# Kernel tuning notes

Measured on AMD Instinct MI355X. Metric: run time of the kernel, lower is better.

## Reference

```python
import jax, jax.numpy as jnp
import numpy as np
from jax import lax

# ReplicationPad1d (left,right) per kernel size, matching Python round((ks-1)/2)
PADS = {2: (0, 1), 3: (1, 1), 6: (2, 3), 12: (6, 5)}

B, N, T, C, OC, E = 8, 1024, 64, 16, 16, 16384


def setup_inputs() -> dict:
    key = jax.random.key(0)
    ks = jax.random.split(key, 16)

    def wn(k, shape, fan_in):
        return jax.random.normal(k, shape, jnp.float32) / jnp.sqrt(jnp.float32(fan_in))

    inp = {
        "x": jax.random.normal(ks[0], (B, N, T, C), jnp.float32),
        "edge_index": jax.random.randint(ks[1], (2, E), 0, N, dtype=jnp.int32),
        # temporal conv branches (Conv1d: [out_ch, in_ch, ks])
        "w_t2": wn(ks[2], (OC, C, 2), C * 2), "b_t2": jnp.zeros((OC,), jnp.float32),
        "w_t3": wn(ks[3], (OC, C, 3), C * 3), "b_t3": jnp.zeros((OC,), jnp.float32),
        "w_t6": wn(ks[4], (OC, C, 6), C * 6), "b_t6": jnp.zeros((OC,), jnp.float32),
        "w_t12": wn(ks[5], (OC, C, 12), C * 12), "b_t12": jnp.zeros((OC,), jnp.float32),
        # GCNConv: lin weight [out, in] (no bias in lin), separate bias
        "w_gcn": wn(ks[6], (OC, C), C), "b_gcn": jnp.zeros((OC,), jnp.float32),
        # slin: Linear(T -> T)
        "w_slin": wn(ks[7], (T, T), T), "b_slin": jnp.zeros((T,), jnp.float32),
    }
    return inp


def reference(x, edge_index, w_t2, b_t2, w_t3, b_t3, w_t6, b_t6, w_t12, b_t12,
              w_gcn, b_gcn, w_slin, b_slin):
    Bd, Nd, Td, Cd = x.shape
    # ---- temporal multi-scale Conv1d branches ----
    xt = x.reshape(Bd * Nd, Td, Cd).transpose(0, 2, 1)  # [BN, C, T]
    outs = []
    for w, b in ((w_t2, b_t2), (w_t3, b_t3), (w_t6, b_t6), (w_t12, b_t12)):
        kern = w.shape[-1]
        l, r = PADS[kern]
        xp = jnp.pad(xt, ((0, 0), (0, 0), (l, r)), mode="edge")  # replication pad
        y = lax.conv_general_dilated(xp, w, (1,), "VALID",
                                     dimension_numbers=("NCH", "OIH", "NCH"))
        outs.append((y + b[None, :, None]).transpose(0, 2, 1))  # [BN, T, OC]
    out_t = jnp.concatenate(outs, axis=-1).reshape(Bd, Nd, Td, -1)  # [B,N,T,4*OC]

    # ---- GCNConv spatial branch (gather-transform-scatter) ----
    xs = x.transpose(0, 2, 1, 3)                         # [B,T,N,C]
    xl = jnp.einsum("btnc,oc->btno", xs, w_gcn)          # [B,T,N,OC]
    row, col = edge_index[0], edge_index[1]
    deg = jnp.zeros((Nd,), x.dtype).at[col].add(1.0) + 1.0  # +1 self loop
    dinv = lax.rsqrt(deg)
    norm = dinv[row] * dinv[col]                         # [E]
    msgs = xl[:, :, row, :] * norm[None, None, :, None]  # gather [B,T,E,OC]
    agg = jnp.zeros_like(xl).at[:, :, col, :].add(msgs)  # scatter-add
    agg = agg + (dinv * dinv)[None, None, :, None] * xl + b_gcn  # self loops + bias

    xs_out = agg.transpose(0, 2, 3, 1)                   # [B,N,OC,T]
    xs_out = jnp.einsum("bnot,st->bnos", xs_out, w_slin) + b_slin
    xs_out = xs_out.transpose(0, 1, 3, 2)                # [B,N,T,OC]

    return jnp.tanh(jnp.concatenate([out_t, xs_out], axis=-1))  # [B,N,T,embed_dim]
```

## Files before the change

kernel.cpp:

```cpp
#include <hip/hip_runtime.h>
#include <hip/hip_bf16.h>

#define BB  8
#define NN  1024
#define TT  64
#define CC  16
#define OCC 16
#define EE  16384
#define CHO 80

typedef float  f32x4  __attribute__((ext_vector_type(4)));
typedef __bf16 bf16x8 __attribute__((ext_vector_type(8)));

static __device__ __forceinline__ float tanh_fast(float v) {
    float e = __expf(2.0f * v);
    return 1.0f - 2.0f * __builtin_amdgcn_rcpf(e + 1.0f);
}
static __device__ __forceinline__ unsigned pk_bf16(float a, float b) {
    unsigned short lo = __builtin_bit_cast(unsigned short, (__bf16)a);
    unsigned short hi = __builtin_bit_cast(unsigned short, (__bf16)b);
    return (unsigned)lo | ((unsigned)hi << 16);
}
static __device__ __forceinline__ float bflo(unsigned u) { return __uint_as_float(u << 16); }
static __device__ __forceinline__ float bfhi(unsigned u) { return __uint_as_float(u & 0xFFFF0000u); }

static __device__ __forceinline__ void acc8(float* ac, int base, float w, float4 v) {
    unsigned ux = __float_as_uint(v.x), uy = __float_as_uint(v.y);
    unsigned uz = __float_as_uint(v.z), uw = __float_as_uint(v.w);
    ac[base + 0] = fmaf(w, bflo(ux), ac[base + 0]);
    ac[base + 1] = fmaf(w, bfhi(ux), ac[base + 1]);
    ac[base + 2] = fmaf(w, bflo(uy), ac[base + 2]);
    ac[base + 3] = fmaf(w, bfhi(uy), ac[base + 3]);
    ac[base + 4] = fmaf(w, bflo(uz), ac[base + 4]);
    ac[base + 5] = fmaf(w, bfhi(uz), ac[base + 5]);
    ac[base + 6] = fmaf(w, bflo(uw), ac[base + 6]);
    ac[base + 7] = fmaf(w, bfhi(uw), ac[base + 7]);
}


__global__ __launch_bounds__(1024) void k_prep(
    const int* __restrict__ ei, const float* __restrict__ x,
    const float* __restrict__ w2,  const float* __restrict__ b2,
    const float* __restrict__ w3,  const float* __restrict__ b3,
    const float* __restrict__ w6,  const float* __restrict__ b6,
    const float* __restrict__ w12, const float* __restrict__ b12,
    const float* __restrict__ wg,  const float* __restrict__ bg,
    const float* __restrict__ wsl,
    int* __restrict__ offg, int* __restrict__ cntg, float* __restrict__ dinvg,
    int* __restrict__ src, float* __restrict__ wE,
    float* __restrict__ wgT, float* __restrict__ bgp, float* __restrict__ bcat,
    __bf16* __restrict__ wslh, __bf16* __restrict__ wsll, __bf16* __restrict__ wtg,
    __bf16* __restrict__ xb) {
    int tid = threadIdx.x, bid = blockIdx.x;
    const float* wsrc[4] = {w2, w3, w6, w12};
    const float* bsrc[4] = {b2, b3, b6, b12};
    const int ksA[4] = {2, 3, 6, 12};
    const int plA[4] = {0, 1, 2, 6};
    if (bid >= 14) {
        int e4 = (bid - 14) * 1024 + tid;
        float4 u = ((const float4*)x)[e4];
        uint2 w;
        w.x = pk_bf16(u.x, u.y);
        w.y = pk_bf16(u.z, u.w);
        ((uint2*)xb)[e4] = w;
        return;
    }
    if (bid == 13) {
        if (tid < 256) wgT[tid] = wg[(tid & 15) * CC + (tid >> 4)];
        else if (tid < 272) bgp[tid - 256] = bg[tid - 256];
        else if (tid < 336) { int j = tid - 272; bcat[j] = bsrc[j >> 4][j & 15]; }
        for (int e = tid; e < 4096; e += 1024) {
            float v = wsl[e];
            __bf16 h = (__bf16)v;
            wslh[e] = h;
            wsll[e] = (__bf16)(v - (float)h);
        }
        return;
    }
    if (bid != 0) {
        int e = (bid - 1) * 1024 + tid;
        int j = e / 192, kk = e - j * 192;
        int d = kk >> 4, c = kk & 15;
        int br = j >> 4, oc = j & 15;
        int k = d - 6 + plA[br];
        float v = (k >= 0 && k < ksA[br]) ? wsrc[br][oc * (CC * ksA[br]) + c * ksA[br] + k] : 0.0f;
        wtg[e] = (__bf16)v;
        return;
    }
    __shared__ int   h[NN];
    __shared__ int   sc[NN];
    __shared__ int   cur[NN];
    __shared__ float dl[NN];
    h[tid] = 0;
    __syncthreads();
    for (int e = tid; e < EE; e += 1024) atomicAdd(&h[ei[EE + e]], 1);
    __syncthreads();
    int v = h[tid];
    sc[tid] = v;
    __syncthreads();
    for (int d = 1; d < NN; d <<= 1) {
        int add = (tid >= d) ? sc[tid - d] : 0;
        __syncthreads();
        sc[tid] += add;
        __syncthreads();
    }
    int oex = sc[tid] - v;
    float dv = rsqrtf((float)v + 1.0f);
    offg[tid] = oex; cntg[tid] = v; dinvg[tid] = dv;
    cur[tid] = oex; dl[tid] = dv;
    __syncthreads();
    for (int e = tid; e < EE; e += 1024) {
        int r = ei[e], c = ei[EE + e];
        int i = atomicAdd(&cur[c], 1);
        src[i] = r;
        wE[i]  = dl[r] * dl[c];
    }
}


__global__ __launch_bounds__(256) void k_main(
    const __bf16* __restrict__ xb, const __bf16* __restrict__ wtg,
    const float* __restrict__ bcat,
    const int* __restrict__ off, const int* __restrict__ cnt,
    const int* __restrict__ src, const float* __restrict__ wE, const float* __restrict__ dinv,
    const float* __restrict__ wgT, const float* __restrict__ bgp,
    const __bf16* __restrict__ wslh, const __bf16* __restrict__ wsll,
    const float* __restrict__ bsl, float* __restrict__ out) {
    __shared__ __align__(16) char smem[18432];
    int tid = threadIdx.x;
    int wave = tid >> 6, lane = tid & 63;
    int l15 = lane & 15, g = lane >> 4;
    int bq = blockIdx.x & 7, nq = blockIdx.x >> 3;
    int n = nq * 4 + wave;
    const __bf16* xbb = xb + (size_t)bq * NN * (TT * CC);

    bf16x8 afr[6];
#pragma unroll
    for (int s = 0; s < 6; s++) {
        const __bf16* p = wtg + (wave * 16 + l15) * 192 + s * 32 + g * 8;
        afr[s] = __builtin_bit_cast(bf16x8, *(const float4*)p);
    }
    float4 bias = *(const float4*)(bcat + wave * 16 + g * 4);

    {
        int t = tid >> 2, c0 = (tid & 3) * 4;
#pragma unroll
        for (int node = 0; node < 4; node++) {
            __bf16* xsn = (__bf16*)(smem + node * 3648);
            uint2 w = *(const uint2*)(xbb + (size_t)(nq * 4 + node) * (TT * CC) + tid * 4);
            *(uint2*)(xsn + (t + 6) * 24 + c0) = w;
            if (t == 0) {
#pragma unroll
                for (int r = 0; r < 6; r++) *(uint2*)(xsn + r * 24 + c0) = w;
            }
            if (t == 63) {
#pragma unroll
                for (int r = 70; r < 76; r++) *(uint2*)(xsn + r * 24 + c0) = w;
            }
        }
    }
    __syncthreads();

    for (int node = 0; node < 4; node++) {
        const __bf16* xsn = (const __bf16*)(smem + node * 3648);
        size_t bn = (size_t)bq * NN + nq * 4 + node;
        f32x4 acc[4];
#pragma unroll
        for (int m = 0; m < 4; m++) acc[m] = (f32x4){bias.x, bias.y, bias.z, bias.w};
#pragma unroll
        for (int m = 0; m < 4; m++) {
#pragma unroll
            for (int s = 0; s < 6; s++) {
                const __bf16* p = xsn + (m * 16 + l15 + 2 * s + (g >> 1)) * 24 + (g & 1) * 8;
                bf16x8 b = __builtin_bit_cast(bf16x8, *(const float4*)p);
                acc[m] = __builtin_amdgcn_mfma_f32_16x16x32_bf16(afr[s], b, acc[m], 0, 0, 0);
            }
        }
#pragma unroll
        for (int m = 0; m < 4; m++) {
            float4 o;
            o.x = tanh_fast(acc[m][0]); o.y = tanh_fast(acc[m][1]);
            o.z = tanh_fast(acc[m][2]); o.w = tanh_fast(acc[m][3]);
            *(float4*)(out + (bn * TT + m * 16 + l15) * CHO + wave * 16 + g * 4) = o;
        }
    }

    float ac[16];
    {
        int o0 = off[n], cn_ = cnt[n];
        float d = dinv[n], d2 = d * d;
        const __bf16* st = xbb + (size_t)n * (TT * CC) + lane * 16;
        float4 s0 = *(const float4*)st;
        float4 s1 = *(const float4*)(st + 8);
        {
            unsigned ux = __float_as_uint(s0.x), uy = __float_as_uint(s0.y);
            unsigned uz = __float_as_uint(s0.z), uw = __float_as_uint(s0.w);
            ac[0] = d2 * bflo(ux); ac[1] = d2 * bfhi(ux);
            ac[2] = d2 * bflo(uy); ac[3] = d2 * bfhi(uy);
            ac[4] = d2 * bflo(uz); ac[5] = d2 * bfhi(uz);
            ac[6] = d2 * bflo(uw); ac[7] = d2 * bfhi(uw);
            ux = __float_as_uint(s1.x); uy = __float_as_uint(s1.y);
            uz = __float_as_uint(s1.z); uw = __float_as_uint(s1.w);
            ac[8]  = d2 * bflo(ux); ac[9]  = d2 * bfhi(ux);
            ac[10] = d2 * bflo(uy); ac[11] = d2 * bfhi(uy);
            ac[12] = d2 * bflo(uz); ac[13] = d2 * bfhi(uz);
            ac[14] = d2 * bflo(uw); ac[15] = d2 * bfhi(uw);
        }
        const int* srcp = src + o0;
        const float* wEp = wE + o0;
        int j = 0;
        for (; j + 4 <= cn_; j += 4) {
            int sA = srcp[j], sB = srcp[j + 1], sC = srcp[j + 2], sD = srcp[j + 3];
            float wA = wEp[j], wB = wEp[j + 1], wC = wEp[j + 2], wD = wEp[j + 3];
            const __bf16* pa = xbb + (size_t)sA * (TT * CC) + lane * 16;
            const __bf16* pb = xbb + (size_t)sB * (TT * CC) + lane * 16;
            const __bf16* pc = xbb + (size_t)sC * (TT * CC) + lane * 16;
            const __bf16* pd = xbb + (size_t)sD * (TT * CC) + lane * 16;
            float4 a0 = *(const float4*)pa, a1 = *(const float4*)(pa + 8);
            float4 b0 = *(const float4*)pb, b1 = *(const float4*)(pb + 8);
            float4 c0 = *(const float4*)pc, c1 = *(const float4*)(pc + 8);
            float4 d0 = *(const float4*)pd, d1 = *(const float4*)(pd + 8);
            acc8(ac, 0, wA, a0); acc8(ac, 8, wA, a1);
            acc8(ac, 0, wB, b0); acc8(ac, 8, wB, b1);
            acc8(ac, 0, wC, c0); acc8(ac, 8, wC, c1);
            acc8(ac, 0, wD, d0); acc8(ac, 8, wD, d1);
        }
        for (; j < cn_; j++) {
            int sA = srcp[j];
            float wA = wEp[j];
            const __bf16* pa = xbb + (size_t)sA * (TT * CC) + lane * 16;
            float4 a0 = *(const float4*)pa, a1 = *(const float4*)(pa + 8);
            acc8(ac, 0, wA, a0); acc8(ac, 8, wA, a1);
        }
    }

    float pv[16];
#pragma unroll
    for (int o = 0; o < 16; o++) {
        float p = bgp[o];
#pragma unroll
        for (int c = 0; c < 16; c++) p = fmaf(wgT[c * 16 + o], ac[c], p);
        pv[o] = p;
    }
    __syncthreads();

    {
        __bf16* xhn = (__bf16*)(smem + wave * 4608);
        __bf16* xln = (__bf16*)(smem + wave * 4608 + 2304);
#pragma unroll
        for (int o = 0; o < 16; o++) {
            __bf16 h = (__bf16)pv[o];
            xhn[o * 72 + lane] = h;
            xln[o * 72 + lane] = (__bf16)(pv[o] - (float)h);
        }
    }
    __syncthreads();

    int sglob = wave * 16 + l15;
    bf16x8 bh[2], bl[2];
#pragma unroll
    for (int k = 0; k < 2; k++) {
        bh[k] = __builtin_bit_cast(bf16x8, *(const float4*)(wslh + sglob * 64 + k * 32 + g * 8));
        bl[k] = __builtin_bit_cast(bf16x8, *(const float4*)(wsll + sglob * 64 + k * 32 + g * 8));
    }
    float bv = bsl[sglob];
    for (int node = 0; node < 4; node++) {
        const __bf16* xhn = (const __bf16*)(smem + node * 4608);
        const __bf16* xln = (const __bf16*)(smem + node * 4608 + 2304);
        f32x4 acc = (f32x4){bv, bv, bv, bv};
        bf16x8 ah[2], al[2];
#pragma unroll
        for (int k = 0; k < 2; k++) {
            ah[k] = __builtin_bit_cast(bf16x8, *(const float4*)(xhn + l15 * 72 + k * 32 + g * 8));
            al[k] = __builtin_bit_cast(bf16x8, *(const float4*)(xln + l15 * 72 + k * 32 + g * 8));
        }
#pragma unroll
        for (int k = 0; k < 2; k++) {
            acc = __builtin_amdgcn_mfma_f32_16x16x32_bf16(ah[k], bh[k], acc, 0, 0, 0);
            acc = __builtin_amdgcn_mfma_f32_16x16x32_bf16(al[k], bh[k], acc, 0, 0, 0);
            acc = __builtin_amdgcn_mfma_f32_16x16x32_bf16(ah[k], bl[k], acc, 0, 0, 0);
        }
        float4 o4;
        o4.x = tanh_fast(acc[0]); o4.y = tanh_fast(acc[1]);
        o4.z = tanh_fast(acc[2]); o4.w = tanh_fast(acc[3]);
        size_t bn = (size_t)bq * NN + nq * 4 + node;
        *(float4*)(out + (bn * TT + sglob) * CHO + 64 + g * 4) = o4;
    }
}


extern "C" void kernel_launch(void* const* d_in, const int* in_sizes, int n_in,
                              void* d_out, int out_size, void* d_ws, size_t ws_size,
                              hipStream_t stream) {
    const float* x   = (const float*)d_in[0];
    const int*   ei  = (const int*)d_in[1];
    const float* w2  = (const float*)d_in[2];
    const float* b2  = (const float*)d_in[3];
    const float* w3  = (const float*)d_in[4];
    const float* b3  = (const float*)d_in[5];
    const float* w6  = (const float*)d_in[6];
    const float* b6  = (const float*)d_in[7];
    const float* w12 = (const float*)d_in[8];
    const float* b12 = (const float*)d_in[9];
    const float* wg  = (const float*)d_in[10];
    const float* bg  = (const float*)d_in[11];
    const float* wsl = (const float*)d_in[12];
    const float* bsl = (const float*)d_in[13];
    float* out = (float*)d_out;

    char*   ws   = (char*)d_ws;
    int*    off  = (int*)(ws);
    int*    cnt  = (int*)(ws + 4096);
    float*  dinv = (float*)(ws + 8192);
    int*    src  = (int*)(ws + 12288);
    float*  wE   = (float*)(ws + 77824);
    float*  wgT  = (float*)(ws + 143360);
    float*  bgp  = (float*)(ws + 144384);
    float*  bcat = (float*)(ws + 144448);
    __bf16* wslh = (__bf16*)(ws + 144704);
    __bf16* wsll = (__bf16*)(ws + 152896);
    __bf16* wtg  = (__bf16*)(ws + 161088);
    __bf16* xb   = (__bf16*)(ws + 4194304);

    k_prep<<<2062, 1024, 0, stream>>>(ei, x, w2, b2, w3, b3, w6, b6, w12, b12, wg, bg, wsl,
                                      off, cnt, dinv, src, wE, wgT, bgp, bcat,
                                      wslh, wsll, wtg, xb);
    k_main<<<BB * NN / 4, 256, 0, stream>>>(xb, wtg, bcat, off, cnt, src, wE, dinv,
                                            wgT, bgp, wslh, wsll, bsl, out);
}
```

Before: 94.87 us.

## Specialize warps: run temporal conv and GCN gather concurrently in 512-thread blocks

Doubles the block to 8 waves and gives each group its own job. Waves 0-3 stage x and compute the temporal MFMA conv, while waves 4-7 each run one node's GCN neighbor gather and projection at the same time. Shared memory is split into separate buffers so the two phases no longer alias, and the slin MFMA stage is split across all 8 waves, two nodes each. The aim is to overlap latency-bound gather loads with conv compute, at the cost of higher per-block register and LDS pressure and possible imbalance between the two wave groups.

```diff
diff --git a/kernel.cpp b/kernel.cpp
--- a/kernel.cpp
+++ b/kernel.cpp
@@ -118,7 +118,7 @@
 }
 
 
-__global__ __launch_bounds__(256) void k_main(
+__global__ __launch_bounds__(512) void k_main(
     const __bf16* __restrict__ xb, const __bf16* __restrict__ wtg,
     const float* __restrict__ bcat,
     const int* __restrict__ off, const int* __restrict__ cnt,
@@ -126,137 +126,128 @@
     const float* __restrict__ wgT, const float* __restrict__ bgp,
     const __bf16* __restrict__ wslh, const __bf16* __restrict__ wsll,
     const float* __restrict__ bsl, float* __restrict__ out) {
-    __shared__ __align__(16) char smem[18432];
+    __shared__ __align__(16) __bf16 xs[4][76 * 24];
+    __shared__ __align__(16) __bf16 xh[4][16 * 72];
+    __shared__ __align__(16) __bf16 xl2[4][16 * 72];
     int tid = threadIdx.x;
-    int wave = tid >> 6, lane = tid & 63;
+    int wid = tid >> 6, lane = tid & 63;
     int l15 = lane & 15, g = lane >> 4;
     int bq = blockIdx.x & 7, nq = blockIdx.x >> 3;
-    int n = nq * 4 + wave;
     const __bf16* xbb = xb + (size_t)bq * NN * (TT * CC);
 
-    bf16x8 afr[6];
-#pragma unroll
-    for (int s = 0; s < 6; s++) {
-        const __bf16* p = wtg + (wave * 16 + l15) * 192 + s * 32 + g * 8;
-        afr[s] = __builtin_bit_cast(bf16x8, *(const float4*)p);
-    }
-    float4 bias = *(const float4*)(bcat + wave * 16 + g * 4);
-
-    {
+    if (wid < 4) {
         int t = tid >> 2, c0 = (tid & 3) * 4;
 #pragma unroll
         for (int node = 0; node < 4; node++) {
-            __bf16* xsn = (__bf16*)(smem + node * 3648);
             uint2 w = *(const uint2*)(xbb + (size_t)(nq * 4 + node) * (TT * CC) + tid * 4);
-            *(uint2*)(xsn + (t + 6) * 24 + c0) = w;
+            *(uint2*)(xs[node] + (t + 6) * 24 + c0) = w;
             if (t == 0) {
 #pragma unroll
-                for (int r = 0; r < 6; r++) *(uint2*)(xsn + r * 24 + c0) = w;
+                for (int r = 0; r < 6; r++) *(uint2*)(xs[node] + r * 24 + c0) = w;
             }
             if (t == 63) {
 #pragma unroll
-                for (int r = 70; r < 76; r++) *(uint2*)(xsn + r * 24 + c0) = w;
-            }
-        }
-    }
-    __syncthreads();
-
-    for (int node = 0; node < 4; node++) {
-        const __bf16* xsn = (const __bf16*)(smem + node * 3648);
-        size_t bn = (size_t)bq * NN + nq * 4 + node;
-        f32x4 acc[4];
-#pragma unroll
-        for (int m = 0; m < 4; m++) acc[m] = (f32x4){bias.x, bias.y, bias.z, bias.w};
-#pragma unroll
-        for (int m = 0; m < 4; m++) {
-#pragma unroll
-            for (int s = 0; s < 6; s++) {
-                const __bf16* p = xsn + (m * 16 + l15 + 2 * s + (g >> 1)) * 24 + (g & 1) * 8;
-                bf16x8 b = __builtin_bit_cast(bf16x8, *(const float4*)p);
-                acc[m] = __builtin_amdgcn_mfma_f32_16x16x32_bf16(afr[s], b, acc[m], 0, 0, 0);
-            }
-        }
-#pragma unroll
-        for (int m = 0; m < 4; m++) {
-            float4 o;
-            o.x = tanh_fast(acc[m][0]); o.y = tanh_fast(acc[m][1]);
-            o.z = tanh_fast(acc[m][2]); o.w = tanh_fast(acc[m][3]);
-            *(float4*)(out + (bn * TT + m * 16 + l15) * CHO + wave * 16 + g * 4) = o;
-        }
-    }
-
-    float ac[16];
-    {
-        int o0 = off[n], cn_ = cnt[n];
-        float d = dinv[n], d2 = d * d;
-        const __bf16* st = xbb + (size_t)n * (TT * CC) + lane * 16;
-        float4 s0 = *(const float4*)st;
-        float4 s1 = *(const float4*)(st + 8);
+                for (int r = 70; r < 76; r++) *(uint2*)(xs[node] + r * 24 + c0) = w;
+            }
+        }
+    }
+    __syncthreads();
+
+    if (wid < 4) {
+        bf16x8 afr[6];
+#pragma unroll
+        for (int s = 0; s < 6; s++) {
+            const __bf16* p = wtg + (wid * 16 + l15) * 192 + s * 32 + g * 8;
+            afr[s] = __builtin_bit_cast(bf16x8, *(const float4*)p);
+        }
+        float4 bias = *(const float4*)(bcat + wid * 16 + g * 4);
+        for (int node = 0; node < 4; node++) {
+            size_t bn = (size_t)bq * NN + nq * 4 + node;
+            f32x4 acc[4];
+#pragma unroll
+            for (int m = 0; m < 4; m++) acc[m] = (f32x4){bias.x, bias.y, bias.z, bias.w};
+#pragma unroll
+            for (int m = 0; m < 4; m++) {
+#pragma unroll
+                for (int s = 0; s < 6; s++) {
+                    const __bf16* p = xs[node] + (m * 16 + l15 + 2 * s + (g >> 1)) * 24 + (g & 1) * 8;
+                    bf16x8 b = __builtin_bit_cast(bf16x8, *(const float4*)p);
+                    acc[m] = __builtin_amdgcn_mfma_f32_16x16x32_bf16(afr[s], b, acc[m], 0, 0, 0);
+                }
+            }
+#pragma unroll
+            for (int m = 0; m < 4; m++) {
+                float4 o;
+                o.x = tanh_fast(acc[m][0]); o.y = tanh_fast(acc[m][1]);
+                o.z = tanh_fast(acc[m][2]); o.w = tanh_fast(acc[m][3]);
+                *(float4*)(out + (bn * TT + m * 16 + l15) * CHO + wid * 16 + g * 4) = o;
+            }
+        }
+    } else {
+        int node = wid - 4;
+        int n = nq * 4 + node;
+        float ac[16];
         {
-            unsigned ux = __float_as_uint(s0.x), uy = __float_as_uint(s0.y);
-            unsigned uz = __float_as_uint(s0.z), uw = __float_as_uint(s0.w);
-            ac[0] = d2 * bflo(ux); ac[1] = d2 * bfhi(ux);
-            ac[2] = d2 * bflo(uy); ac[3] = d2 * bfhi(uy);
-            ac[4] = d2 * bflo(uz); ac[5] = d2 * bfhi(uz);
-            ac[6] = d2 * bflo(uw); ac[7] = d2 * bfhi(uw);
-            ux = __float_as_uint(s1.x); uy = __float_as_uint(s1.y);
-            uz = __float_as_uint(s1.z); uw = __float_as_uint(s1.w);
-            ac[8]  = d2 * bflo(ux); ac[9]  = d2 * bfhi(ux);
-            ac[10] = d2 * bflo(uy); ac[11] = d2 * bfhi(uy);
-            ac[12] = d2 * bflo(uz); ac[13] = d2 * bfhi(uz);
-            ac[14] = d2 * bflo(uw); ac[15] = d2 * bfhi(uw);
-        }
-        const int* srcp = src + o0;
-        const float* wEp = wE + o0;
-        int j = 0;
-        for (; j + 4 <= cn_; j += 4) {
-            int sA = srcp[j], sB = srcp[j + 1], sC = srcp[j + 2], sD = srcp[j + 3];
-            float wA = wEp[j], wB = wEp[j + 1], wC = wEp[j + 2], wD = wEp[j + 3];
-            const __bf16* pa = xbb + (size_t)sA * (TT * CC) + lane * 16;
-            const __bf16* pb = xbb + (size_t)sB * (TT * CC) + lane * 16;
-            const __bf16* pc = xbb + (size_t)sC * (TT * CC) + lane * 16;
-            const __bf16* pd = xbb + (size_t)sD * (TT * CC) + lane * 16;
-            float4 a0 = *(const float4*)pa, a1 = *(const float4*)(pa + 8);
-            float4 b0 = *(const float4*)pb, b1 = *(const float4*)(pb + 8);
-            float4 c0 = *(const float4*)pc, c1 = *(const float4*)(pc + 8);
-            float4 d0 = *(const float4*)pd, d1 = *(const float4*)(pd + 8);
-            acc8(ac, 0, wA, a0); acc8(ac, 8, wA, a1);
-            acc8(ac, 0, wB, b0); acc8(ac, 8, wB, b1);
-            acc8(ac, 0, wC, c0); acc8(ac, 8, wC, c1);
-            acc8(ac, 0, wD, d0); acc8(ac, 8, wD, d1);
-        }
-        for (; j < cn_; j++) {
-            int sA = srcp[j];
-            float wA = wEp[j];
-            const __bf16* pa = xbb + (size_t)sA * (TT * CC) + lane * 16;
-            float4 a0 = *(const float4*)pa, a1 = *(const float4*)(pa + 8);
-            acc8(ac, 0, wA, a0); acc8(ac, 8, wA, a1);
-        }
-    }
-
-    float pv[16];
-#pragma unroll
-    for (int o = 0; o < 16; o++) {
-        float p = bgp[o];
-#pragma unroll
-        for (int c = 0; c < 16; c++) p = fmaf(wgT[c * 16 + o], ac[c], p);
-        pv[o] = p;
-    }
-    __syncthreads();
-
-    {
-        __bf16* xhn = (__bf16*)(smem + wave * 4608);
-        __bf16* xln = (__bf16*)(smem + wave * 4608 + 2304);
+            int o0 = off[n], cn_ = cnt[n];
+            float d = dinv[n], d2 = d * d;
+            const __bf16* st = xbb + (size_t)n * (TT * CC) + lane * 16;
+            float4 s0 = *(const float4*)st;
+            float4 s1 = *(const float4*)(st + 8);
+            {
+                unsigned ux = __float_as_uint(s0.x), uy = __float_as_uint(s0.y);
+                unsigned uz = __float_as_uint(s0.z), uw = __float_as_uint(s0.w);
+                ac[0] = d2 * bflo(ux); ac[1] = d2 * bfhi(ux);
+                ac[2] = d2 * bflo(uy); ac[3] = d2 * bfhi(uy);
+                ac[4] = d2 * bflo(uz); ac[5] = d2 * bfhi(uz);
+                ac[6] = d2 * bflo(uw); ac[7] = d2 * bfhi(uw);
+                ux = __float_as_uint(s1.x); uy = __float_as_uint(s1.y);
+                uz = __float_as_uint(s1.z); uw = __float_as_uint(s1.w);
+                ac[8]  = d2 * bflo(ux); ac[9]  = d2 * bfhi(ux);
+                ac[10] = d2 * bflo(uy); ac[11] = d2 * bfhi(uy);
+                ac[12] = d2 * bflo(uz); ac[13] = d2 * bfhi(uz);
+                ac[14] = d2 * bflo(uw); ac[15] = d2 * bfhi(uw);
+            }
+            const int* srcp = src + o0;
+            const float* wEp = wE + o0;
+            int j = 0;
+            for (; j + 4 <= cn_; j += 4) {
+                int sA = srcp[j], sB = srcp[j + 1], sC = srcp[j + 2], sD = srcp[j + 3];
+                float wA = wEp[j], wB = wEp[j + 1], wC = wEp[j + 2], wD = wEp[j + 3];
+                const __bf16* pa = xbb + (size_t)sA * (TT * CC) + lane * 16;
+                const __bf16* pb = xbb + (size_t)sB * (TT * CC) + lane * 16;
+                const __bf16* pc = xbb + (size_t)sC * (TT * CC) + lane * 16;
+                const __bf16* pd = xbb + (size_t)sD * (TT * CC) + lane * 16;
+                float4 a0 = *(const float4*)pa, a1 = *(const float4*)(pa + 8);
+                float4 b0 = *(const float4*)pb, b1 = *(const float4*)(pb + 8);
+                float4 c0 = *(const float4*)pc, c1 = *(const float4*)(pc + 8);
+                float4 d0 = *(const float4*)pd, d1 = *(const float4*)(pd + 8);
+                acc8(ac, 0, wA, a0); acc8(ac, 8, wA, a1);
+                acc8(ac, 0, wB, b0); acc8(ac, 8, wB, b1);
+                acc8(ac, 0, wC, c0); acc8(ac, 8, wC, c1);
+                acc8(ac, 0, wD, d0); acc8(ac, 8, wD, d1);
+            }
+            for (; j < cn_; j++) {
+                int sA = srcp[j];
+                float wA = wEp[j];
+                const __bf16* pa = xbb + (size_t)sA * (TT * CC) + lane * 16;
+                float4 a0 = *(const float4*)pa, a1 = *(const float4*)(pa + 8);
+                acc8(ac, 0, wA, a0); acc8(ac, 8, wA, a1);
+            }
+        }
 #pragma unroll
         for (int o = 0; o < 16; o++) {
-            __bf16 h = (__bf16)pv[o];
-            xhn[o * 72 + lane] = h;
-            xln[o * 72 + lane] = (__bf16)(pv[o] - (float)h);
-        }
-    }
-    __syncthreads();
-
-    int sglob = wave * 16 + l15;
+            float p = bgp[o];
+#pragma unroll
+            for (int c = 0; c < 16; c++) p = fmaf(wgT[c * 16 + o], ac[c], p);
+            __bf16 h = (__bf16)p;
+            xh[node][o * 72 + lane]  = h;
+            xl2[node][o * 72 + lane] = (__bf16)(p - (float)h);
+        }
+    }
+    __syncthreads();
+
+    int q = wid & 3;
+    int sglob = q * 16 + l15;
     bf16x8 bh[2], bl[2];
 #pragma unroll
     for (int k = 0; k < 2; k++) {
@@ -264,15 +255,15 @@
         bl[k] = __builtin_bit_cast(bf16x8, *(const float4*)(wsll + sglob * 64 + k * 32 + g * 8));
     }
     float bv = bsl[sglob];
-    for (int node = 0; node < 4; node++) {
-        const __bf16* xhn = (const __bf16*)(smem + node * 4608);
-        const __bf16* xln = (const __bf16*)(smem + node * 4608 + 2304);
+#pragma unroll
+    for (int nn = 0; nn < 2; nn++) {
+        int node = (wid >> 2) * 2 + nn;
         f32x4 acc = (f32x4){bv, bv, bv, bv};
         bf16x8 ah[2], al[2];
 #pragma unroll
         for (int k = 0; k < 2; k++) {
-            ah[k] = __builtin_bit_cast(bf16x8, *(const float4*)(xhn + l15 * 72 + k * 32 + g * 8));
-            al[k] = __builtin_bit_cast(bf16x8, *(const float4*)(xln + l15 * 72 + k * 32 + g * 8));
+            ah[k] = __builtin_bit_cast(bf16x8, *(const float4*)(xh[node]  + l15 * 72 + k * 32 + g * 8));
+            al[k] = __builtin_bit_cast(bf16x8, *(const float4*)(xl2[node] + l15 * 72 + k * 32 + g * 8));
         }
 #pragma unroll
         for (int k = 0; k < 2; k++) {
@@ -325,6 +316,6 @@
     k_prep<<<2062, 1024, 0, stream>>>(ei, x, w2, b2, w3, b3, w6, b6, w12, b12, wg, bg, wsl,
                                       off, cnt, dinv, src, wE, wgT, bgp, bcat,
                                       wslh, wsll, wtg, xb);
-    k_main<<<BB * NN / 4, 256, 0, stream>>>(xb, wtg, bcat, off, cnt, src, wE, dinv,
+    k_main<<<BB * NN / 4, 512, 0, stream>>>(xb, wtg, bcat, off, cnt, src, wE, dinv,
                                             wgT, bgp, wslh, wsll, bsl, out);
 }
```

After: 99.81 us. 1.05x slower.
